# Optimization experiments

Hardware: AMD Instinct MI355X
Metric: run time of the kernel (lower is better)

## Reference

```python
import jax, jax.numpy as jnp
import numpy as np

B, C, W, H = 32, 256, 32, 32


def setup_inputs() -> dict:
    key = jax.random.key(0)
    ks = jax.random.split(key, 9)
    s = 1.0 / np.sqrt(C)
    return {
        "x": jax.random.normal(ks[0], (B, C, W, H), dtype=jnp.float32),
        "Wq": jax.random.normal(ks[1], (C, C), dtype=jnp.float32) * s,
        "bq": jax.random.normal(ks[2], (C,), dtype=jnp.float32) * 0.01,
        "Wk": jax.random.normal(ks[3], (C, C), dtype=jnp.float32) * s,
        "bk": jax.random.normal(ks[4], (C,), dtype=jnp.float32) * 0.01,
        "Wv": jax.random.normal(ks[5], (C, C), dtype=jnp.float32) * s,
        "bv": jax.random.normal(ks[6], (C,), dtype=jnp.float32) * 0.01,
        "rel_h": jax.random.normal(ks[7], (1, C, 1, H), dtype=jnp.float32),
        "rel_w": jax.random.normal(ks[8], (1, C, W, 1), dtype=jnp.float32),
    }


def reference(x, Wq, bq, Wk, bk, Wv, bv, rel_h, rel_w):
    b, c, w, h = x.shape
    n = w * h
    xf = x.reshape(b, c, n)  # [B, C, N]
    # 1x1 conv == channel-mixing matmul (out_ch 'o' from in_ch 'c')
    q = jnp.einsum('oc,bcn->bon', Wq, xf) + bq[None, :, None]
    k = jnp.einsum('oc,bcn->bon', Wk, xf) + bk[None, :, None]
    v = jnp.einsum('oc,bcn->bon', Wv, xf) + bv[None, :, None]
    # content-content: q^T k -> [B, N, N]
    content_content = jnp.einsum('bci,bcj->bij', q, k)
    # relative position bias: (rel_h + rel_w) broadcasts to [1, C, W, H]
    rel = (rel_h + rel_w).reshape(c, n)  # [C, N]
    content_position = jnp.einsum('cp,bcj->bpj', rel, q)  # [B, N, N]
    attention = jax.nn.softmax(content_content + content_position, axis=-1)
    # out[b,c,i] = sum_j v[b,c,j] * attention[b,i,j]
    out = jnp.einsum('bcj,bij->bci', v, attention)
    return out.reshape(b, c, w, h)
```

## Files before the change

kernel.cpp:

```cpp
#include <hip/hip_runtime.h>


#define NB 32
#define NC 256
#define NNN 1024

typedef _Float16 f16;
typedef __attribute__((ext_vector_type(8))) _Float16 half8;
typedef __attribute__((ext_vector_type(4))) float f32x4;
typedef __attribute__((ext_vector_type(4))) float float4v;

__device__ __forceinline__ f32x4 mfma16(half8 a, half8 b, f32x4 c) {
  return __builtin_amdgcn_mfma_f32_16x16x32_f16(a, b, c, 0, 0, 0);
}
__device__ __forceinline__ void gload16(const f16* g, f16* l) {
  __builtin_amdgcn_global_load_lds(
      (const __attribute__((address_space(1))) void*)g,
      (__attribute__((address_space(3))) void*)l, 16, 0, 0);
}

__global__ __launch_bounds__(256) void k_prep(
    const float* __restrict__ Wq, const float* __restrict__ Wk,
    const float* __restrict__ Wv, const float* __restrict__ relh,
    const float* __restrict__ relw, f16* __restrict__ Wh, f16* __restrict__ RT) {
  int bid = blockIdx.x, tid = threadIdx.x;
  if (bid < 192) {
    int base = (bid * 256 + tid) * 4;
    int w = base >> 16, j = base & 65535;
    const float* src = (w == 0) ? Wq : ((w == 1) ? Wk : Wv);
    float4v v = *(const float4v*)(src + j);
    Wh[base + 0] = (f16)v.x; Wh[base + 1] = (f16)v.y;
    Wh[base + 2] = (f16)v.z; Wh[base + 3] = (f16)v.w;
  } else {
    int n = bid - 192;
    int c = tid;
    RT[n * NC + c] = (f16)(relw[c * 32 + (n >> 5)] + relh[c * 32 + (n & 31)]);
  }
}

__global__ __launch_bounds__(256) void k_xpose(
    const float* __restrict__ x, f16* __restrict__ xT) {
  int bid = blockIdx.x;
  int nt = bid & 15, ct = (bid >> 4) & 3, b = bid >> 6;
  int c0 = ct << 6, n0 = nt << 6;
  __shared__ f16 T[64][72];
  int t = threadIdx.x;
  {
    int cl = t >> 2, n4 = (t & 3) << 4;
    const float* src = x + ((size_t)(b * NC + c0 + cl) << 10) + n0 + n4;
    float4v v0 = *(const float4v*)(src + 0);
    float4v v1 = *(const float4v*)(src + 4);
    float4v v2 = *(const float4v*)(src + 8);
    float4v v3 = *(const float4v*)(src + 12);
    f16* d = &T[cl][n4];
    d[0]=(f16)v0.x; d[1]=(f16)v0.y; d[2]=(f16)v0.z; d[3]=(f16)v0.w;
    d[4]=(f16)v1.x; d[5]=(f16)v1.y; d[6]=(f16)v1.z; d[7]=(f16)v1.w;
    d[8]=(f16)v2.x; d[9]=(f16)v2.y; d[10]=(f16)v2.z; d[11]=(f16)v2.w;
    d[12]=(f16)v3.x; d[13]=(f16)v3.y; d[14]=(f16)v3.z; d[15]=(f16)v3.w;
  }
  __syncthreads();
  {
    int nl = t >> 2, c16 = (t & 3) << 4;
    half8 h0, h1;
    #pragma unroll
    for (int u = 0; u < 8; ++u) h0[u] = T[c16 + u][nl];
    #pragma unroll
    for (int u = 0; u < 8; ++u) h1[u] = T[c16 + 8 + u][nl];
    f16* dst = xT + ((size_t)(b * NNN + n0 + nl) << 8) + c0 + c16;
    *(half8*)(dst) = h0;
    *(half8*)(dst + 8) = h1;
  }
}

__global__ __launch_bounds__(256, 4) void k_proj(
    const f16* __restrict__ xT, const f16* __restrict__ Wh,
    const float* __restrict__ bq, const float* __restrict__ bk,
    const float* __restrict__ bv,
    f16* __restrict__ KQ, f16* __restrict__ V) {
  int b = blockIdx.x >> 4;
  int n0 = (blockIdx.x & 15) << 6;
  int tid = threadIdx.x;
  int wave = tid >> 6, lane = tid & 63;
  int lq = lane & 15, g = lane >> 4;
  int ow = wave << 6;
  const f16* xTb = xT + ((size_t)(b * NNN + n0) << 8);

  __shared__ f16 XS[64][256];

  {
    int li = lane & 31;
    #pragma unroll
    for (int q2 = 0; q2 < 8; ++q2) {
      int r2 = wave * 16 + q2 * 2;
      int r = r2 + (lane >> 5);
      int slot = (li & 0x10) | ((li ^ (r & 15)) & 0xF);
      gload16(xTb + ((size_t)r << 8) + slot * 8, &XS[r2][0]);
    }
  }
  asm volatile("s_waitcnt vmcnt(0)" ::: "memory");
  __syncthreads();

  #pragma unroll 1
  for (int which = 0; which < 2; ++which) {
    const f16* Wp = Wh + which * 65536;
    const float* bias = which ? bk : bq;
    int koff = which ? 0 : 256;
    f32x4 acc[4][4];
    #pragma unroll
    for (int f = 0; f < 4; ++f) {
      float bf = bias[ow + 16 * f + lq];
      #pragma unroll
      for (int mm = 0; mm < 4; ++mm) acc[mm][f] = (f32x4){bf, bf, bf, bf};
    }
    #pragma unroll
    for (int kk = 0; kk < 8; ++kk) {
      int cb = kk * 32 + 8 * g;
      int s = 4 * kk + g;
      int p = (s & 0x10) | ((s ^ lq) & 0xF);
      half8 xa[4], wb[4];
      #pragma unroll
      for (int mm = 0; mm < 4; ++mm)
        xa[mm] = *(const half8*)(&XS[16 * mm + lq][p * 8]);
      #pragma unroll
      for (int f = 0; f < 4; ++f)
        wb[f] = *(const half8*)(Wp + (size_t)(ow + 16 * f + lq) * NC + cb);
      #pragma unroll
      for (int mm = 0; mm < 4; ++mm)
        #pragma unroll
        for (int f = 0; f < 4; ++f)
          acc[mm][f] = mfma16(xa[mm], wb[f], acc[mm][f]);
    }
    #pragma unroll
    for (int mm = 0; mm < 4; ++mm)
      #pragma unroll
      for (int f = 0; f < 4; ++f)
        #pragma unroll
        for (int r = 0; r < 4; ++r)
          KQ[((size_t)(b * NNN + n0 + 16 * mm + 4 * g + r) << 9) + koff + ow + 16 * f + lq] =
              (f16)acc[mm][f][r];
  }

  {
    const f16* Wp = Wh + 2 * 65536;
    f32x4 acc[4][4];
    #pragma unroll
    for (int mm = 0; mm < 4; ++mm)
      #pragma unroll
      for (int r = 0; r < 4; ++r) {
        float bf = bv[ow + 16 * mm + 4 * g + r];
        #pragma unroll
        for (int f = 0; f < 4; ++f) acc[mm][f][r] = bf;
      }
    #pragma unroll
    for (int kk = 0; kk < 8; ++kk) {
      int cb = kk * 32 + 8 * g;
      int s = 4 * kk + g;
      int p = (s & 0x10) | ((s ^ lq) & 0xF);
      half8 va[4], xb2[4];
      #pragma unroll
      for (int mm = 0; mm < 4; ++mm)
        va[mm] = *(const half8*)(Wp + (size_t)(ow + 16 * mm + lq) * NC + cb);
      #pragma unroll
      for (int f = 0; f < 4; ++f)
        xb2[f] = *(const half8*)(&XS[16 * f + lq][p * 8]);
      #pragma unroll
      for (int mm = 0; mm < 4; ++mm)
        #pragma unroll
        for (int f = 0; f < 4; ++f)
          acc[mm][f] = mfma16(va[mm], xb2[f], acc[mm][f]);
    }
    #pragma unroll
    for (int mm = 0; mm < 4; ++mm)
      #pragma unroll
      for (int f = 0; f < 4; ++f)
        #pragma unroll
        for (int r = 0; r < 4; ++r)
          V[((size_t)(b * NC + ow + 16 * mm + 4 * g + r) << 10) + n0 + 16 * f + lq] =
              (f16)acc[mm][f][r];
  }
}

__global__ __launch_bounds__(256, 2) void k_flash5(
    const f16* __restrict__ KQ, const f16* __restrict__ V,
    const f16* __restrict__ RT, float* __restrict__ out) {
  int bid = blockIdx.x;
  int swz = (bid & 7) * 64 + (bid >> 3);
  int b = swz >> 4;
  int i0 = (swz & 15) << 6;
  int tid = threadIdx.x;
  int wave = tid >> 6, lane = tid & 63;
  int lq = lane & 15, g = lane >> 4;
  int iw = i0 + 16 * wave;

  __shared__ f16 KQS[2][2][16][512];

  const f16* KQb = KQ + ((size_t)b << 19);
  const f16* Vb = V + ((size_t)b << 18);

  half8 QA[16];
  #pragma unroll
  for (int kk = 0; kk < 8; ++kk)
    QA[kk] = *(const half8*)(KQb + ((size_t)(iw + lq) << 9) + 256 + kk * 32 + 8 * g);
  #pragma unroll
  for (int kk = 0; kk < 8; ++kk)
    QA[8 + kk] = *(const half8*)(RT + (size_t)(iw + lq) * NC + kk * 32 + 8 * g);

  f32x4 acc[16];
  #pragma unroll
  for (int cf = 0; cf < 16; ++cf) acc[cf] = (f32x4){0.f, 0.f, 0.f, 0.f};
  float m = -1e30f, lsum = 0.f;

#define STAGE(JT, BUF)                                                        \
  {                                                                           \
    _Pragma("unroll")                                                         \
    for (int pp = 0; pp < 2; ++pp) {                                          \
      _Pragma("unroll")                                                       \
      for (int q = 0; q < 4; ++q) {                                           \
        int rho_ = 4 * wave + q;                                              \
        int j_ = (JT) * 32 + 8 * wave + 4 * pp + q;                           \
        int slot_ = (lane & 0x30) | ((lane ^ rho_) & 0xF);                    \
        gload16(KQb + ((size_t)j_ << 9) + slot_ * 8, &KQS[BUF][pp][rho_][0]); \
      }                                                                       \
    }                                                                         \
  }

  STAGE(0, 0);
  asm volatile("s_waitcnt vmcnt(0)" ::: "memory");
  __syncthreads();

  #pragma unroll 1
  for (int jt = 0; jt < 32; ++jt) {
    int cur = jt & 1;
    if (jt < 31) {
      if (cur) STAGE(jt + 1, 0) else STAGE(jt + 1, 1);
    }
    f32x4 S0 = (f32x4){0.f, 0.f, 0.f, 0.f};
    f32x4 S1 = (f32x4){0.f, 0.f, 0.f, 0.f};
    const f16* B0 = &KQS[cur][0][lq][0];
    const f16* B1 = &KQS[cur][1][lq][0];
    __builtin_amdgcn_s_setprio(1);
    #pragma unroll
    for (int kk = 0; kk < 16; ++kk) {
      int s = 4 * kk + g;
      int ps = (s & 0x30) | ((s ^ lq) & 0xF);
      S0 = mfma16(*(const half8*)(B0 + ps * 8), QA[kk], S0);
      S1 = mfma16(*(const half8*)(B1 + ps * 8), QA[kk], S1);
    }
    __builtin_amdgcn_s_setprio(0);

    float tmax = fmaxf(fmaxf(fmaxf(S0[0], S0[1]), fmaxf(S0[2], S0[3])),
                       fmaxf(fmaxf(S1[0], S1[1]), fmaxf(S1[2], S1[3])));
    tmax = fmaxf(tmax, __shfl_xor(tmax, 16));
    tmax = fmaxf(tmax, __shfl_xor(tmax, 32));
    bool grow = tmax > m + 8.f;
    if (__builtin_amdgcn_ballot_w64(grow)) {
      float mn = fmaxf(m, tmax);
      float sc = __expf(m - mn);
      m = mn;
      lsum *= sc;
      #pragma unroll
      for (int cf = 0; cf < 16; ++cf) {
        acc[cf][0] *= sc; acc[cf][1] *= sc; acc[cf][2] *= sc; acc[cf][3] *= sc;
      }
    }
    float p0 = __expf(S0[0] - m), p1 = __expf(S0[1] - m),
          p2 = __expf(S0[2] - m), p3 = __expf(S0[3] - m);
    float p4 = __expf(S1[0] - m), p5 = __expf(S1[1] - m),
          p6 = __expf(S1[2] - m), p7 = __expf(S1[3] - m);
    lsum += ((p0 + p1) + (p2 + p3)) + ((p4 + p5) + (p6 + p7));
    half8 pa;
    pa[0] = (f16)p0; pa[1] = (f16)p1; pa[2] = (f16)p2; pa[3] = (f16)p3;
    pa[4] = (f16)p4; pa[5] = (f16)p5; pa[6] = (f16)p6; pa[7] = (f16)p7;

    size_t j0 = (size_t)(jt * 32 + 8 * g);
    __builtin_amdgcn_s_setprio(1);
    #pragma unroll
    for (int cf = 0; cf < 16; ++cf) {
      half8 vv = *(const half8*)(Vb + ((size_t)(16 * cf + lq) << 10) + j0);
      acc[cf] = mfma16(vv, pa, acc[cf]);
    }
    __builtin_amdgcn_s_setprio(0);

    asm volatile("s_waitcnt vmcnt(0)" ::: "memory");
    __syncthreads();
  }
#undef STAGE

  lsum += __shfl_xor(lsum, 16);
  lsum += __shfl_xor(lsum, 32);
  float li = 1.f / lsum;
  #pragma unroll
  for (int cf = 0; cf < 16; ++cf)
    #pragma unroll
    for (int r = 0; r < 4; ++r)
      out[((size_t)(b * NC + 16 * cf + 4 * g + r) << 10) + iw + lq] = acc[cf][r] * li;
}

extern "C" void kernel_launch(void* const* d_in, const int* in_sizes, int n_in,
                              void* d_out, int out_size, void* d_ws, size_t ws_size,
                              hipStream_t stream) {
  const float* x = (const float*)d_in[0];
  const float* Wq = (const float*)d_in[1];
  const float* bq = (const float*)d_in[2];
  const float* Wk = (const float*)d_in[3];
  const float* bk = (const float*)d_in[4];
  const float* Wv = (const float*)d_in[5];
  const float* bv = (const float*)d_in[6];
  const float* relh = (const float*)d_in[7];
  const float* relw = (const float*)d_in[8];

  char* ws = (char*)d_ws;
  const size_t MB = 1 << 20;
  f16* xT = (f16*)(ws);
  f16* KQ = (f16*)(ws + 16 * MB);
  f16* V  = (f16*)(ws + 48 * MB);
  f16* RT = (f16*)(ws + 64 * MB);
  f16* Wh = (f16*)(ws + 64 * MB + 512 * 1024);

  k_prep<<<dim3(1216), dim3(256), 0, stream>>>(Wq, Wk, Wv, relh, relw, Wh, RT);
  k_xpose<<<dim3(2048), dim3(256), 0, stream>>>(x, xT);
  k_proj<<<dim3(512), dim3(256), 0, stream>>>(xT, Wh, bq, bk, bv, KQ, V);
  k_flash5<<<dim3(512), dim3(256), 0, stream>>>(KQ, V, RT, (float*)d_out);
}
```

Baseline: 320.8 us.

## Stage projection outputs through LDS for coalesced stores; prefetch V and defer max reduction

```diff
diff --git a/kernel.cpp b/kernel.cpp
--- a/kernel.cpp
+++ b/kernel.cpp
@@ -72,7 +72,7 @@
   }
 }
 
-__global__ __launch_bounds__(256, 4) void k_proj(
+__global__ __launch_bounds__(256, 2) void k_proj(
     const f16* __restrict__ xT, const f16* __restrict__ Wh,
     const float* __restrict__ bq, const float* __restrict__ bk,
     const float* __restrict__ bv,
@@ -86,6 +86,7 @@
   const f16* xTb = xT + ((size_t)(b * NNN + n0) << 8);
 
   __shared__ f16 XS[64][256];
+  __shared__ f16 BB[18432];
 
   {
     int li = lane & 31;
@@ -130,14 +131,22 @@
         for (int f = 0; f < 4; ++f)
           acc[mm][f] = mfma16(xa[mm], wb[f], acc[mm][f]);
     }
+    __syncthreads();
     #pragma unroll
     for (int mm = 0; mm < 4; ++mm)
       #pragma unroll
       for (int f = 0; f < 4; ++f)
         #pragma unroll
         for (int r = 0; r < 4; ++r)
-          KQ[((size_t)(b * NNN + n0 + 16 * mm + 4 * g + r) << 9) + koff + ow + 16 * f + lq] =
-              (f16)acc[mm][f][r];
+          BB[(16 * mm + 4 * g + r) * 272 + ow + 16 * f + lq] = (f16)acc[mm][f][r];
+    __syncthreads();
+    #pragma unroll
+    for (int it = 0; it < 8; ++it) {
+      int row = wave * 16 + it * 2 + (lane >> 5);
+      int cc = (lane & 31) * 8;
+      half8 v = *(const half8*)(&BB[row * 272 + cc]);
+      *(half8*)(&KQ[((size_t)(b * NNN + n0 + row) << 9) + koff + cc]) = v;
+    }
   }
 
   {
@@ -169,18 +178,26 @@
         for (int f = 0; f < 4; ++f)
           acc[mm][f] = mfma16(va[mm], xb2[f], acc[mm][f]);
     }
+    __syncthreads();
     #pragma unroll
     for (int mm = 0; mm < 4; ++mm)
       #pragma unroll
       for (int f = 0; f < 4; ++f)
         #pragma unroll
         for (int r = 0; r < 4; ++r)
-          V[((size_t)(b * NC + ow + 16 * mm + 4 * g + r) << 10) + n0 + 16 * f + lq] =
-              (f16)acc[mm][f][r];
-  }
-}
-
-__global__ __launch_bounds__(256, 2) void k_flash5(
+          BB[(ow + 16 * mm + 4 * g + r) * 72 + 16 * f + lq] = (f16)acc[mm][f][r];
+    __syncthreads();
+    #pragma unroll
+    for (int it = 0; it < 8; ++it) {
+      int o = wave * 64 + it * 8 + (lane >> 3);
+      int cc = (lane & 7) * 8;
+      half8 v = *(const half8*)(&BB[o * 72 + cc]);
+      *(half8*)(&V[((size_t)(b * NC + o) << 10) + n0 + cc]) = v;
+    }
+  }
+}
+
+__global__ __launch_bounds__(256, 2) void k_flash6(
     const f16* __restrict__ KQ, const f16* __restrict__ V,
     const f16* __restrict__ RT, float* __restrict__ out) {
   int bid = blockIdx.x;
@@ -248,12 +265,19 @@
     }
     __builtin_amdgcn_s_setprio(0);
 
-    float tmax = fmaxf(fmaxf(fmaxf(S0[0], S0[1]), fmaxf(S0[2], S0[3])),
+    size_t j0 = (size_t)(jt * 32 + 8 * g);
+    half8 vpre[8];
+    #pragma unroll
+    for (int cf = 0; cf < 8; ++cf)
+      vpre[cf] = *(const half8*)(Vb + ((size_t)(16 * cf + lq) << 10) + j0);
+
+    float pmax = fmaxf(fmaxf(fmaxf(S0[0], S0[1]), fmaxf(S0[2], S0[3])),
                        fmaxf(fmaxf(S1[0], S1[1]), fmaxf(S1[2], S1[3])));
-    tmax = fmaxf(tmax, __shfl_xor(tmax, 16));
-    tmax = fmaxf(tmax, __shfl_xor(tmax, 32));
-    bool grow = tmax > m + 8.f;
+    bool grow = pmax > m + 8.f;
     if (__builtin_amdgcn_ballot_w64(grow)) {
+      float tmax = pmax;
+      tmax = fmaxf(tmax, __shfl_xor(tmax, 16));
+      tmax = fmaxf(tmax, __shfl_xor(tmax, 32));
       float mn = fmaxf(m, tmax);
       float sc = __expf(m - mn);
       m = mn;
@@ -272,10 +296,12 @@
     pa[0] = (f16)p0; pa[1] = (f16)p1; pa[2] = (f16)p2; pa[3] = (f16)p3;
     pa[4] = (f16)p4; pa[5] = (f16)p5; pa[6] = (f16)p6; pa[7] = (f16)p7;
 
-    size_t j0 = (size_t)(jt * 32 + 8 * g);
     __builtin_amdgcn_s_setprio(1);
     #pragma unroll
-    for (int cf = 0; cf < 16; ++cf) {
+    for (int cf = 0; cf < 8; ++cf)
+      acc[cf] = mfma16(vpre[cf], pa, acc[cf]);
+    #pragma unroll
+    for (int cf = 8; cf < 16; ++cf) {
       half8 vv = *(const half8*)(Vb + ((size_t)(16 * cf + lq) << 10) + j0);
       acc[cf] = mfma16(vv, pa, acc[cf]);
     }
@@ -320,5 +346,5 @@
   k_prep<<<dim3(1216), dim3(256), 0, stream>>>(Wq, Wk, Wv, relh, relw, Wh, RT);
   k_xpose<<<dim3(2048), dim3(256), 0, stream>>>(x, xT);
   k_proj<<<dim3(512), dim3(256), 0, stream>>>(xT, Wh, bq, bk, bv, KQ, V);
-  k_flash5<<<dim3(512), dim3(256), 0, stream>>>(KQ, V, RT, (float*)d_out);
-}
+  k_flash6<<<dim3(512), dim3(256), 0, stream>>>(KQ, V, RT, (float*)d_out);
+}
```

Measured after the change: 327.4 us. +2.1%, slower.
